# Kernel optimization log

Hardware: AMD Instinct MI355X
Metric: run time of the kernel (lower is better)

The kernel has to match this reference:

```python
import jax, jax.numpy as jnp
import numpy as np

B, C, H, W = 128, 8, 144, 144
TW, OG = 5, 2          # token_window, off_grid
NCLS, DT = 6, 256      # num_cls, dim_token
ITC = C * H * TW       # in_token_channel = 5760
EPS = 1e-5


def setup_inputs() -> dict:
    key = jax.random.key(0)
    ks = jax.random.split(key, 40)
    n = jax.random.normal
    u = jax.random.uniform
    CW = C * W  # 1152
    inp = {
        'x': n(ks[0], (B, C, H, W), jnp.float32),
        # ext head: Conv1d(1152,256,1) -> BN(256) -> Conv1d(256,2,1)
        'ext_w1': n(ks[1], (256, CW)) * 0.02, 'ext_b1': jnp.zeros((256,)),
        'ext_g': jnp.ones((256,)), 'ext_bb': jnp.zeros((256,)),
        'ext_m': n(ks[2], (256,)) * 0.1, 'ext_v': u(ks[3], (256,), minval=0.5, maxval=1.5),
        'ext_w2': n(ks[4], (2, 256)) * 0.05, 'ext_b2': jnp.zeros((2,)),
        # cls head: Conv1d(1152,256,1) -> BN(256) -> Conv1d(256,144,1)
        'cls_w1': n(ks[5], (256, CW)) * 0.02, 'cls_b1': jnp.zeros((256,)),
        'cls_g': jnp.ones((256,)), 'cls_bb': jnp.zeros((256,)),
        'cls_m': n(ks[6], (256,)) * 0.1, 'cls_v': u(ks[7], (256,), minval=0.5, maxval=1.5),
        'cls_w2': n(ks[8], (W, 256)) * 0.05, 'cls_b2': jnp.zeros((W,)),
        # to_token Linear(5760,256) and class embeddings
        'tok_w': n(ks[9], (ITC, DT)) * 0.01, 'tok_b': jnp.zeros((DT,)),
        'emb': n(ks[10], (NCLS, DT)),
        # transformer (depth=1, heads=2, dim_head=32 -> inner=64)
        'ln1_g': jnp.ones((DT,)), 'ln1_b': jnp.zeros((DT,)),
        'qkv_w': n(ks[11], (DT, 3 * 64)) * 0.05,
        'out_w': n(ks[12], (64, DT)) * 0.05, 'out_b': jnp.zeros((DT,)),
        'ln2_g': jnp.ones((DT,)), 'ln2_b': jnp.zeros((DT,)),
        'ff_w1': n(ks[13], (DT, 512)) * 0.05, 'ff_b1': jnp.zeros((512,)),
        'ff_w2': n(ks[14], (512, DT)) * 0.05, 'ff_b2': jnp.zeros((DT,)),
        'lnf_g': jnp.ones((DT,)), 'lnf_b': jnp.zeros((DT,)),
        'fin_w': n(ks[15], (DT, ITC)) * 0.02, 'fin_b': jnp.zeros((ITC,)),
    }
    return inp


def _ln(z, g, b):
    mu = jnp.mean(z, -1, keepdims=True)
    var = jnp.var(z, -1, keepdims=True)
    return (z - mu) * jax.lax.rsqrt(var + EPS) * g + b


def reference(x, ext_w1, ext_b1, ext_g, ext_bb, ext_m, ext_v, ext_w2, ext_b2,
              cls_w1, cls_b1, cls_g, cls_bb, cls_m, cls_v, cls_w2, cls_b2,
              tok_w, tok_b, emb,
              ln1_g, ln1_b, qkv_w, out_w, out_b,
              ln2_g, ln2_b, ff_w1, ff_b1, ff_w2, ff_b2,
              lnf_g, lnf_b, fin_w, fin_b):

    def head(row, w1, b1, g, bet, m, v, w2, b2):
        # row: [B, C*W, H]; 1x1 conv = per-position GEMM, BN in eval mode
        h = jnp.einsum('oc,bch->boh', w1, row) + b1[:, None]
        h = (h - m[:, None]) * jax.lax.rsqrt(v[:, None] + EPS) * g[:, None] + bet[:, None]
        h = jnp.einsum('oc,bch->boh', w2, h) + b2[:, None]
        return jnp.transpose(h, (0, 2, 1))  # [B, H, out]

    def heads_on(xx):
        # 'b c h w -> b (c w) h' (c major, w minor)
        row = jnp.transpose(xx, (0, 1, 3, 2)).reshape(B, C * W, H)
        e = jax.nn.softmax(head(row, ext_w1, ext_b1, ext_g, ext_bb, ext_m, ext_v, ext_w2, ext_b2), axis=2)
        c = jax.nn.softmax(head(row, cls_w1, cls_b1, cls_g, cls_bb, cls_m, cls_v, cls_w2, cls_b2), axis=2)
        return e, c

    ext, cls = heads_on(x)
    xp = jnp.pad(x, ((0, 0), (0, 0), (0, 0), (OG, OG)))  # [B,C,H,W+4]

    argmax_col = jnp.argmax(cls, axis=2)                  # [B,H]
    idx = argmax_col[:, :, None] + jnp.arange(TW)         # window in padded coords

    def transformer(t):  # t: [B, N, DT]
        z = _ln(t, ln1_g, ln1_b)
        q, k, v = jnp.split(z @ qkv_w, 3, axis=-1)
        sp = lambda a: a.reshape(B, -1, 2, 32).transpose(0, 2, 1, 3)  # b h n d
        q, k, v = sp(q), sp(k), sp(v)
        att = jax.nn.softmax(jnp.einsum('bhnd,bhmd->bhnm', q, k) * (32 ** -0.5), axis=-1)
        o = jnp.einsum('bhnm,bhmd->bhnd', att, v).transpose(0, 2, 1, 3).reshape(B, -1, 64)
        t = o @ out_w + out_b + t
        z = _ln(t, ln2_g, ln2_b)
        t = jax.nn.gelu(z @ ff_w1 + ff_b1, approximate=False) @ ff_w2 + ff_b2 + t
        t = _ln(t, lnf_g, lnf_b)
        return (t @ fin_w + fin_b).reshape(B, -1, C, H, TW)  # [B,N,C,H,TW]

    def refine(xpad):
        g_idx = jnp.broadcast_to(idx[:, None], (B, C, H, TW))
        patches = jnp.take_along_axis(xpad, g_idx, axis=3)    # [B,C,H,TW]
        tok = patches.reshape(B, -1) @ tok_w + tok_b          # [B,DT]
        tokens = tok[:, None, :] + emb[None]                  # [B,NCLS,DT]
        refined = transformer(tokens)                         # [B,NCLS,C,H,TW]
        xpt = jnp.transpose(xpad, (0, 2, 3, 1))               # [B,H,Wp,C]
        bb = jnp.arange(B)[:, None, None]
        hh = jnp.arange(H)[None, :, None]
        for i in range(NCLS):
            xpt = xpt.at[bb, hh, idx].set(jnp.transpose(refined[:, i], (0, 2, 3, 1)))
        return jnp.transpose(xpt, (0, 3, 1, 2))

    xp = jax.lax.cond(jnp.mean(ext[:, :, 0]) > 0.3, refine, lambda a: a, xp)
    x2 = xp[:, :, :, OG:W + OG]
    ext2, cls2 = heads_on(x2)
    return ext, cls, ext2, cls2
```

## Files before the change

### kernel.cpp

```cpp
#include <hip/hip_runtime.h>
#include <math.h>

#define EPSF 1e-5f
#define GAPTH 2e-4f
#define NKS 2
#define KSL 576
#define RROWS 18432


typedef __attribute__((ext_vector_type(8))) short short8v;
typedef __attribute__((ext_vector_type(4))) float f32x4;
typedef unsigned short ushort;
typedef unsigned int uint;

__device__ inline ushort f2bf(float f) {
    uint u = __float_as_uint(f);
    uint r = (u + 0x7FFFu + ((u >> 16) & 1u)) >> 16;
    return (ushort)r;
}
__device__ inline float bf2f(ushort h) { return __uint_as_float(((uint)h) << 16); }

__global__ __launch_bounds__(256) void wcomb_build(
    const float* __restrict__ w1e, const float* __restrict__ b1e, const float* __restrict__ ge,
    const float* __restrict__ bbe, const float* __restrict__ me, const float* __restrict__ ve,
    const float* __restrict__ w2e, const float* __restrict__ b2e,
    const float* __restrict__ w1c, const float* __restrict__ b1c, const float* __restrict__ gc,
    const float* __restrict__ bbc, const float* __restrict__ mc, const float* __restrict__ vc,
    const float* __restrict__ w2c, const float* __restrict__ b2c,
    float* __restrict__ Wc32, ushort* __restrict__ Wchi, ushort* __restrict__ Wclo,
    float* __restrict__ cconst)
{
    __shared__ float coef[256];
    __shared__ float csum[4];
    const int j = blockIdx.x, kq = blockIdx.y, tid = threadIdx.x;
    const int lane = tid & 63, wid = tid >> 6;

    const float *w1 = nullptr, *w2row = nullptr, *b1 = nullptr, *g = nullptr,
                *bb = nullptr, *m = nullptr, *v = nullptr;
    float b2v = 0.f;
    int valid = 0;
    if (j < 144) {
        valid = 1; w1 = w1c; w2row = w2c + (size_t)j * 256;
        b1 = b1c; g = gc; bb = bbc; m = mc; v = vc; b2v = b2c[j];
    } else if (j < 146) {
        valid = 1; w1 = w1e; w2row = w2e + (size_t)(j - 144) * 256;
        b1 = b1e; g = ge; bb = bbe; m = me; v = ve; b2v = b2e[j - 144];
    }

    float cf = 0.f, cc = 0.f;
    if (valid) {
        float s = g[tid] * rsqrtf(v[tid] + EPSF);
        float w2v = w2row[tid];
        cf = w2v * s;
        cc = w2v * ((b1[tid] - m[tid]) * s + bb[tid]);
    }
    coef[tid] = cf;
    if (kq == 0) {
        float t = cc;
#pragma unroll
        for (int off = 32; off; off >>= 1) t += __shfl_xor(t, off);
        if (lane == 0) csum[wid] = t;
    }
    __syncthreads();
    if (kq == 0 && tid == 0)
        cconst[j] = valid ? ((csum[0] + csum[1]) + (csum[2] + csum[3]) + b2v) : 0.f;

    for (int k = kq * 288 + tid; k < (kq + 1) * 288; k += 256) {
        float acc = 0.f;
        if (valid) {
            for (int o = 0; o < 256; o++) acc += coef[o] * w1[(size_t)o * 1152 + k];
        }
        Wc32[(size_t)j * 1152 + k] = acc;
        ushort hi = f2bf(acc);
        Wchi[(size_t)j * 1152 + k] = hi;
        Wclo[(size_t)j * 1152 + k] = f2bf(acc - bf2f(hi));
    }
}

__global__ void zero_counters(int* __restrict__ cand_count)
{
    *cand_count = 0;
}

__global__ __launch_bounds__(256) void transpose_w(
    const float* __restrict__ src, float* __restrict__ dst, int R, int Cc)
{
    __shared__ float tile[32][33];
    const int rb = blockIdx.y * 32, cb = blockIdx.x * 32;
    const int tx = threadIdx.x & 31, ty = threadIdx.x >> 5;
#pragma unroll
    for (int i = ty; i < 32; i += 8) {
        int r = rb + i, c = cb + tx;
        tile[i][tx] = (r < R && c < Cc) ? src[(size_t)r * Cc + c] : 0.f;
    }
    __syncthreads();
#pragma unroll
    for (int i = ty; i < 32; i += 8) {
        int c = cb + i, r = rb + tx;
        if (c < Cc && r < R) dst[(size_t)c * R + r] = tile[tx][i];
    }
}

__global__ __launch_bounds__(256) void logits_gemm(
    const float* __restrict__ x, const ushort* __restrict__ Wchi, const ushort* __restrict__ Wclo,
    float* __restrict__ logits_part)
{
    __shared__ ushort Ahi[64][40], Alo[64][40], Bhi[160][40], Blo[160][40];
    const int tid = threadIdx.x;
    const int lane = tid & 63, wid = tid >> 6;
    const int wm = wid & 1, wn = wid >> 1;
    const int rb = blockIdx.x * 64;
    const int ks = blockIdx.y;
    const int kbase = ks * KSL;
    const int NIT = KSL / 32;

    const int rl = tid >> 2, kk = (tid & 3) << 3;
    const int arow = rb + rl;
    const int ab = arow / 144, ahh = arow - ab * 144;

    const int br0 = tid >> 2, bk0 = (tid & 3) << 3;
    const int br2 = 128 + (tid >> 2), bk2 = (tid & 3) << 3;

    float av[8];
    short8v vbh0, vbl0, vbh1, vbl1, vbh2, vbl2;

    auto LOAD = [&](int kb) {
        int k1 = kb + kk, c1 = k1 / 144, w1 = k1 - c1 * 144;
        const float4 t0 = *reinterpret_cast<const float4*>(
            x + (((size_t)(ab * 8 + c1) * 144 + ahh) * 144 + w1));
        const float4 t1 = *reinterpret_cast<const float4*>(
            x + (((size_t)(ab * 8 + c1) * 144 + ahh) * 144 + w1 + 4));
        av[0] = t0.x; av[1] = t0.y; av[2] = t0.z; av[3] = t0.w;
        av[4] = t1.x; av[5] = t1.y; av[6] = t1.z; av[7] = t1.w;
        size_t o0 = (size_t)br0 * 1152 + kb + bk0;
        vbh0 = *reinterpret_cast<const short8v*>(Wchi + o0);
        vbl0 = *reinterpret_cast<const short8v*>(Wclo + o0);
        size_t o1 = (size_t)(br0 + 64) * 1152 + kb + bk0;
        vbh1 = *reinterpret_cast<const short8v*>(Wchi + o1);
        vbl1 = *reinterpret_cast<const short8v*>(Wclo + o1);
        if (tid < 128) {
            size_t o2 = (size_t)br2 * 1152 + kb + bk2;
            vbh2 = *reinterpret_cast<const short8v*>(Wchi + o2);
            vbl2 = *reinterpret_cast<const short8v*>(Wclo + o2);
        }
    };

    auto STORE = [&]() {
        short8v hv, lv;
#pragma unroll
        for (int q = 0; q < 8; q++) {
            ushort h = f2bf(av[q]);
            hv[q] = (short)h;
            lv[q] = (short)f2bf(av[q] - bf2f(h));
        }
        *reinterpret_cast<short8v*>(&Ahi[rl][kk]) = hv;
        *reinterpret_cast<short8v*>(&Alo[rl][kk]) = lv;
        *reinterpret_cast<short8v*>(&Bhi[br0][bk0]) = vbh0;
        *reinterpret_cast<short8v*>(&Blo[br0][bk0]) = vbl0;
        *reinterpret_cast<short8v*>(&Bhi[br0 + 64][bk0]) = vbh1;
        *reinterpret_cast<short8v*>(&Blo[br0 + 64][bk0]) = vbl1;
        if (tid < 128) {
            *reinterpret_cast<short8v*>(&Bhi[br2][bk2]) = vbh2;
            *reinterpret_cast<short8v*>(&Blo[br2][bk2]) = vbl2;
        }
    };

    f32x4 acc[2][5];
#pragma unroll
    for (int mt = 0; mt < 2; mt++)
#pragma unroll
        for (int nt = 0; nt < 5; nt++) acc[mt][nt] = (f32x4){0.f, 0.f, 0.f, 0.f};

    const int fr = lane & 15, fg = (lane >> 4) << 3;

    LOAD(kbase);
    for (int t = 0; t < NIT; t++) {
        STORE();
        if (t < NIT - 1) LOAD(kbase + (t + 1) * 32);
        __syncthreads();
        short8v ah0 = *reinterpret_cast<const short8v*>(&Ahi[wm * 32 + fr][fg]);
        short8v al0 = *reinterpret_cast<const short8v*>(&Alo[wm * 32 + fr][fg]);
        short8v ah1 = *reinterpret_cast<const short8v*>(&Ahi[wm * 32 + 16 + fr][fg]);
        short8v al1 = *reinterpret_cast<const short8v*>(&Alo[wm * 32 + 16 + fr][fg]);
#pragma unroll
        for (int nt = 0; nt < 5; nt++) {
            short8v bh = *reinterpret_cast<const short8v*>(&Bhi[wn * 80 + nt * 16 + fr][fg]);
            short8v bl = *reinterpret_cast<const short8v*>(&Blo[wn * 80 + nt * 16 + fr][fg]);
            acc[0][nt] = __builtin_amdgcn_mfma_f32_16x16x32_bf16(ah0, bh, acc[0][nt], 0, 0, 0);
            acc[0][nt] = __builtin_amdgcn_mfma_f32_16x16x32_bf16(ah0, bl, acc[0][nt], 0, 0, 0);
            acc[0][nt] = __builtin_amdgcn_mfma_f32_16x16x32_bf16(al0, bh, acc[0][nt], 0, 0, 0);
            acc[1][nt] = __builtin_amdgcn_mfma_f32_16x16x32_bf16(ah1, bh, acc[1][nt], 0, 0, 0);
            acc[1][nt] = __builtin_amdgcn_mfma_f32_16x16x32_bf16(ah1, bl, acc[1][nt], 0, 0, 0);
            acc[1][nt] = __builtin_amdgcn_mfma_f32_16x16x32_bf16(al1, bh, acc[1][nt], 0, 0, 0);
        }
        __syncthreads();
    }

    float* base = logits_part + (size_t)ks * RROWS * 160;
#pragma unroll
    for (int mt = 0; mt < 2; mt++) {
#pragma unroll
        for (int nt = 0; nt < 5; nt++) {
            int gcol = wn * 80 + nt * 16 + fr;
            if (gcol < 146) {
                float* dst = base + (size_t)(rb + wm * 32 + mt * 16 + ((lane >> 4) << 2)) * 160 + gcol;
#pragma unroll
                for (int i = 0; i < 4; i++)
                    dst[(size_t)i * 160] = acc[mt][nt][i];
            }
        }
    }
}

template<int DELTA>
__global__ __launch_bounds__(256) void softmax_heads(
    const float* __restrict__ logits_part, const float* __restrict__ cconst,
    float* __restrict__ out_cls, float* __restrict__ out_ext,
    int* __restrict__ amax, float* __restrict__ partials,
    int* __restrict__ cand_count, int* __restrict__ cand_list,
    const float* __restrict__ x, const float* __restrict__ WcT,
    const float* __restrict__ refined5, const int* __restrict__ flag)
{
    __shared__ float ps[4];
    __shared__ float dL[4][148];
    __shared__ float dsh[4][40];
    __shared__ int   ksh[4][40];
    const int r4 = threadIdx.x >> 6, lane = threadIdx.x & 63;
    const int row = blockIdx.x * 4 + r4;

    if (DELTA) {
        const int fl = *flag;
        if (fl) {
            const int b = row / 144, hh = row - b * 144;
            const int a = amax[row];
            if (lane < 40) {
                int c = lane / 5, tw = lane - c * 5;
                int w = a - 2 + tw;
                float d = 0.f; int k = 0;
                if (w >= 0 && w < 144) {
                    k = c * 144 + w;
                    d = refined5[(size_t)b * 5760 + (c * 144 + hh) * 5 + tw]
                      - x[((size_t)(b * 8 + c) * 144 + hh) * 144 + w];
                }
                dsh[r4][lane] = d; ksh[r4][lane] = k;
            }
            __syncthreads();
#pragma unroll
            for (int rj = 0; rj < 3; rj++) {
                int j = lane + rj * 64;
                if (j < 146) {
                    float acc = 0.f;
#pragma unroll 8
                    for (int i = 0; i < 40; i++)
                        acc += WcT[(size_t)ksh[r4][i] * 160 + j] * dsh[r4][i];
                    dL[r4][j] = acc;
                }
            }
        } else {
#pragma unroll
            for (int rj = 0; rj < 3; rj++) {
                int j = lane + rj * 64;
                if (j < 146) dL[r4][j] = 0.f;
            }
        }
        __syncthreads();
    }

    const float* L0 = logits_part + (size_t)row * 160;
    const float* L1 = L0 + (size_t)RROWS * 160;
    float v0 = L0[lane] + L1[lane] + cconst[lane];
    float v1 = L0[lane + 64] + L1[lane + 64] + cconst[lane + 64];
    float v2 = (lane < 16) ? (L0[lane + 128] + L1[lane + 128] + cconst[lane + 128])
                           : -3.0e38f;
    if (DELTA) {
        v0 += dL[r4][lane];
        v1 += dL[r4][lane + 64];
        if (lane < 16) v2 += dL[r4][lane + 128];
    }
    float m = v0; int mi = lane;
    if (v1 > m) { m = v1; mi = lane + 64; }
    if (v2 > m) { m = v2; mi = lane + 128; }
    float m1 = v0, m2 = -3.0e38f;
    if (v1 > m1) { m2 = m1; m1 = v1; } else m2 = v1;
    if (v2 > m1) { m2 = m1; m1 = v2; } else m2 = fmaxf(m2, v2);
#pragma unroll
    for (int off = 32; off; off >>= 1) {
        float om = __shfl_xor(m, off);
        int   oi = __shfl_xor(mi, off);
        if (om > m || (om == m && oi < mi)) { m = om; mi = oi; }
        float om1 = __shfl_xor(m1, off);
        float om2 = __shfl_xor(m2, off);
        float nm1 = fmaxf(m1, om1);
        m2 = fmaxf(fminf(m1, om1), fmaxf(m2, om2));
        m1 = nm1;
    }
    float e0 = expf(v0 - m), e1 = expf(v1 - m);
    float e2 = (lane < 16) ? expf(v2 - m) : 0.f;
    float s = e0 + e1 + e2;
#pragma unroll
    for (int off = 32; off; off >>= 1) s += __shfl_xor(s, off);
    float inv = 1.f / s;
    float* O = out_cls + (size_t)row * 144;
    O[lane] = e0 * inv;
    O[lane + 64] = e1 * inv;
    if (lane < 16) O[lane + 128] = e2 * inv;

    float l0 = L0[144] + L1[144] + cconst[144];
    float l1 = L0[145] + L1[145] + cconst[145];
    if (DELTA) { l0 += dL[r4][144]; l1 += dL[r4][145]; }
    float mx = fmaxf(l0, l1);
    float ee0 = expf(l0 - mx), ee1 = expf(l1 - mx);
    float einv = 1.f / (ee0 + ee1);
    float p0 = ee0 * einv;
    if (lane == 0) {
        out_ext[(size_t)row * 2] = p0;
        out_ext[(size_t)row * 2 + 1] = ee1 * einv;
        if (amax != nullptr && !DELTA) {
            amax[row] = mi;
            if (m1 - m2 < GAPTH) {
                int slot = atomicAdd(cand_count, 1);
                cand_list[slot] = row;
            }
        }
    }
    if (partials != nullptr) {
        if (lane == 0) ps[r4] = p0;
        __syncthreads();
        if (threadIdx.x == 0) partials[blockIdx.x] = (ps[0] + ps[1]) + (ps[2] + ps[3]);
    }
}

__global__ __launch_bounds__(256) void reduce_flag(const float* __restrict__ partials, int n,
                                                   int* __restrict__ flag)
{
    __shared__ float sm[256];
    int tid = threadIdx.x;
    float s = 0.f;
    for (int i = tid; i < n; i += 256) s += partials[i];
    sm[tid] = s; __syncthreads();
    for (int off = 128; off; off >>= 1) {
        if (tid < off) sm[tid] += sm[tid + off];
        __syncthreads();
    }
    if (tid == 0) *flag = (sm[0] * (1.f / 18432.f) > 0.3f) ? 1 : 0;
}

__global__ __launch_bounds__(256) void fixup_list(
    const int* __restrict__ cand_count, const int* __restrict__ cand_list,
    const float* __restrict__ x,
    const float* __restrict__ w1cT, const float* __restrict__ b1c,
    const float* __restrict__ gc, const float* __restrict__ bbc,
    const float* __restrict__ mc, const float* __restrict__ vc,
    const float* __restrict__ w2cT, const float* __restrict__ b2c,
    int* __restrict__ amax)
{
    __shared__ float xrow[1152];
    __shared__ float hsh[256];
    __shared__ float Lsh[144];
    const int tid = threadIdx.x;
    const int n = *cand_count;

    for (int ci = blockIdx.x; ci < n; ci += gridDim.x) {
        const int row = cand_list[ci];
        const int b = row / 144, hh = row - b * 144;
        for (int e = tid; e < 1152; e += 256) {
            int c = e / 144, w = e - c * 144;
            xrow[e] = x[(((size_t)(b * 8 + c) * 144 + hh) * 144) + w];
        }
        __syncthreads();
        {
            float a0 = 0.f, a1 = 0.f, a2 = 0.f, a3 = 0.f;
#pragma unroll 4
            for (int k = 0; k < 1152; k += 4) {
                a0 += w1cT[(size_t)k * 256 + tid] * xrow[k];
                a1 += w1cT[(size_t)(k + 1) * 256 + tid] * xrow[k + 1];
                a2 += w1cT[(size_t)(k + 2) * 256 + tid] * xrow[k + 2];
                a3 += w1cT[(size_t)(k + 3) * 256 + tid] * xrow[k + 3];
            }
            float a = (a0 + a1) + (a2 + a3);
            float sc = gc[tid] * rsqrtf(vc[tid] + EPSF);
            hsh[tid] = (a + b1c[tid] - mc[tid]) * sc + bbc[tid];
        }
        __syncthreads();
        if (tid < 144) {
            float a0 = 0.f, a1 = 0.f, a2 = 0.f, a3 = 0.f;
#pragma unroll 4
            for (int k = 0; k < 256; k += 4) {
                a0 += w2cT[(size_t)k * 144 + tid] * hsh[k];
                a1 += w2cT[(size_t)(k + 1) * 144 + tid] * hsh[k + 1];
                a2 += w2cT[(size_t)(k + 2) * 144 + tid] * hsh[k + 2];
                a3 += w2cT[(size_t)(k + 3) * 144 + tid] * hsh[k + 3];
            }
            Lsh[tid] = (a0 + a1) + (a2 + a3) + b2c[tid];
        }
        __syncthreads();
        if (tid == 0) {
            int bi = 0; float bv = Lsh[0];
            for (int j = 1; j < 144; j++) if (Lsh[j] > bv) { bv = Lsh[j]; bi = j; }
            amax[row] = bi;
        }
        __syncthreads();
    }
}

__global__ __launch_bounds__(256) void tok_partial(const float* __restrict__ x,
    const int* __restrict__ amax, const float* __restrict__ tok_w, float* __restrict__ tpart)
{
    __shared__ float P[720];
    __shared__ int ash[144];
    int b = blockIdx.x, c = blockIdx.y, tid = threadIdx.x;
    if (tid < 144) ash[tid] = amax[b * 144 + tid];
    __syncthreads();
    for (int e = tid; e < 720; e += 256) {
        int hh = e / 5, tw = e - hh * 5;
        int w = ash[hh] + tw - 2;
        P[e] = (w >= 0 && w < 144) ? x[(((size_t)(b * 8 + c) * 144 + hh) * 144) + w] : 0.f;
    }
    __syncthreads();
    const float* wbase = tok_w + (size_t)c * 720 * 256;
    float a0 = 0.f, a1 = 0.f, a2 = 0.f, a3 = 0.f;
    for (int k = 0; k < 720; k += 4) {
        a0 += P[k]     * wbase[(size_t)k * 256 + tid];
        a1 += P[k + 1] * wbase[(size_t)(k + 1) * 256 + tid];
        a2 += P[k + 2] * wbase[(size_t)(k + 2) * 256 + tid];
        a3 += P[k + 3] * wbase[(size_t)(k + 3) * 256 + tid];
    }
    tpart[((size_t)b * 8 + c) * 256 + tid] = (a0 + a1) + (a2 + a3);
}

__global__ __launch_bounds__(512) void attn_front(
    const float* __restrict__ tpart, const float* __restrict__ tok_b,
    const float* __restrict__ emb,
    const float* __restrict__ ln1_g, const float* __restrict__ ln1_b,
    const float* __restrict__ qkv_w,
    const float* __restrict__ out_w, const float* __restrict__ out_b,
    const float* __restrict__ ln2_g, const float* __restrict__ ln2_b,
    float* __restrict__ z2_5, float* __restrict__ t5out)
{
    __shared__ float s[256];
    __shared__ float z[6][256];
    __shared__ float qk[6][192];
    __shared__ float att[2][6];
    __shared__ float o5[64];
    __shared__ float t5[256];
    __shared__ float stat[2];
    const int b = blockIdx.x, tid = threadIdx.x;
    const int lane = tid & 63, wv = tid >> 6;
    const int g4 = tid >> 2, l4 = tid & 3;

    if (tid < 256) {
        float a = tok_b[tid];
#pragma unroll
        for (int ks = 0; ks < 8; ks++) a += tpart[((size_t)b * 8 + ks) * 256 + tid];
        s[tid] = a;
    }
    __syncthreads();

    if (wv < 6) {
        float y[4], s1 = 0.f, s2 = 0.f;
#pragma unroll
        for (int q = 0; q < 4; q++) {
            int k = lane + 64 * q;
            y[q] = s[k] + emb[wv * 256 + k];
            s1 += y[q]; s2 += y[q] * y[q];
        }
#pragma unroll
        for (int off = 32; off; off >>= 1) { s1 += __shfl_xor(s1, off); s2 += __shfl_xor(s2, off); }
        float mu = s1 * (1.f / 256.f);
        float var = s2 * (1.f / 256.f) - mu * mu;
        float rs = rsqrtf(var + EPSF);
#pragma unroll
        for (int q = 0; q < 4; q++) {
            int k = lane + 64 * q;
            z[wv][k] = (y[q] - mu) * rs * ln1_g[k] + ln1_b[k];
        }
    }
    __syncthreads();

    for (int tt = g4; tt < 832; tt += 128) {
        int i, c;
        if (tt < 768) { i = tt >> 7; c = 64 + (tt & 127); }
        else          { i = 5;       c = tt - 768; }
        float a = 0.f;
#pragma unroll 8
        for (int j = 0; j < 64; j++) {
            int k = l4 + 4 * j;
            a += z[i][k] * qkv_w[(size_t)k * 192 + c];
        }
        a += __shfl_xor(a, 1);
        a += __shfl_xor(a, 2);
        if (l4 == 0) qk[i][c] = a;
    }
    __syncthreads();

    if (tid < 12) {
        int h = tid / 6, j = tid - h * 6;
        float a = 0.f;
#pragma unroll
        for (int d = 0; d < 32; d++) a += qk[5][h * 32 + d] * qk[j][64 + h * 32 + d];
        att[h][j] = a * 0.17677669529663687f;
    }
    __syncthreads();
    if (tid < 2) {
        float m = -3.0e38f;
        for (int j = 0; j < 6; j++) m = fmaxf(m, att[tid][j]);
        float ssum = 0.f;
        for (int j = 0; j < 6; j++) { float e = expf(att[tid][j] - m); att[tid][j] = e; ssum += e; }
        float inv = 1.f / ssum;
        for (int j = 0; j < 6; j++) att[tid][j] *= inv;
    }
    __syncthreads();
    if (tid < 64) {
        int h = tid >> 5;
        float a = 0.f;
#pragma unroll
        for (int j = 0; j < 6; j++) a += att[h][j] * qk[j][128 + tid];
        o5[tid] = a;
    }
    __syncthreads();

    for (int tt = g4; tt < 256; tt += 128) {
        float a = 0.f;
#pragma unroll
        for (int j = 0; j < 16; j++) {
            int d = l4 + 4 * j;
            a += o5[d] * out_w[(size_t)d * 256 + tt];
        }
        a += __shfl_xor(a, 1);
        a += __shfl_xor(a, 2);
        if (l4 == 0) t5[tt] = a + out_b[tt] + s[tt] + emb[5 * 256 + tt];
    }
    __syncthreads();

    if (wv == 0) {
        float s1 = 0.f, s2 = 0.f;
#pragma unroll
        for (int q = 0; q < 4; q++) { float vv = t5[lane + 64 * q]; s1 += vv; s2 += vv * vv; }
#pragma unroll
        for (int off = 32; off; off >>= 1) { s1 += __shfl_xor(s1, off); s2 += __shfl_xor(s2, off); }
        if (lane == 0) {
            float mu = s1 * (1.f / 256.f);
            float var = s2 * (1.f / 256.f) - mu * mu;
            stat[0] = mu; stat[1] = rsqrtf(var + EPSF);
        }
    }
    __syncthreads();
    if (tid < 256) {
        t5out[(size_t)b * 256 + tid] = t5[tid];
        z2_5[(size_t)b * 256 + tid] = (t5[tid] - stat[0]) * stat[1] * ln2_g[tid] + ln2_b[tid];
    }
}

__global__ __launch_bounds__(512) void ff1_gelu(
    const float* __restrict__ z2_5, const float* __restrict__ ff_w1,
    const float* __restrict__ ff_b1, float* __restrict__ f5)
{
    __shared__ float zsh[256];
    const int b = blockIdx.x, half = blockIdx.y, tid = threadIdx.x;
    const int g4 = tid >> 2, l4 = tid & 3;
    if (tid < 256) zsh[tid] = z2_5[(size_t)b * 256 + tid];
    __syncthreads();
    for (int tt = g4; tt < 256; tt += 128) {
        const int jj = half * 256 + tt;
        float a = 0.f;
#pragma unroll 8
        for (int j = 0; j < 64; j++) {
            int k = l4 + 4 * j;
            a += zsh[k] * ff_w1[(size_t)k * 512 + jj];
        }
        a += __shfl_xor(a, 1);
        a += __shfl_xor(a, 2);
        if (l4 == 0) {
            a += ff_b1[jj];
            f5[(size_t)b * 512 + jj] = 0.5f * a * (1.f + erff(a * 0.70710678118654752f));
        }
    }
}

__global__ __launch_bounds__(512) void ff2_lnf(
    const float* __restrict__ f5, const float* __restrict__ ff_w2,
    const float* __restrict__ ff_b2, const float* __restrict__ t5in,
    const float* __restrict__ lnf_g, const float* __restrict__ lnf_b,
    float* __restrict__ tfin)
{
    __shared__ float fsh[512];
    __shared__ float tsh[256];
    __shared__ float stat[2];
    const int b = blockIdx.x, tid = threadIdx.x;
    const int lane = tid & 63, wv = tid >> 6;
    const int g4 = tid >> 2, l4 = tid & 3;
    fsh[tid] = f5[(size_t)b * 512 + tid];
    __syncthreads();
    for (int tt = g4; tt < 256; tt += 128) {
        float a = 0.f;
#pragma unroll 8
        for (int j = 0; j < 128; j++) {
            int k = l4 + 4 * j;
            a += fsh[k] * ff_w2[(size_t)k * 256 + tt];
        }
        a += __shfl_xor(a, 1);
        a += __shfl_xor(a, 2);
        if (l4 == 0) tsh[tt] = a + ff_b2[tt] + t5in[(size_t)b * 256 + tt];
    }
    __syncthreads();
    if (wv == 0) {
        float s1 = 0.f, s2 = 0.f;
#pragma unroll
        for (int q = 0; q < 4; q++) { float vv = tsh[lane + 64 * q]; s1 += vv; s2 += vv * vv; }
#pragma unroll
        for (int off = 32; off; off >>= 1) { s1 += __shfl_xor(s1, off); s2 += __shfl_xor(s2, off); }
        if (lane == 0) {
            float mu = s1 * (1.f / 256.f);
            float var = s2 * (1.f / 256.f) - mu * mu;
            stat[0] = mu; stat[1] = rsqrtf(var + EPSF);
        }
    }
    __syncthreads();
    if (tid < 256)
        tfin[(size_t)b * 256 + tid] = (tsh[tid] - stat[0]) * stat[1] * lnf_g[tid] + lnf_b[tid];
}

__global__ __launch_bounds__(256) void fin_gemm(const float* __restrict__ tfin,
    const float* __restrict__ fin_w, const float* __restrict__ fin_b, float* __restrict__ refined5)
{
    __shared__ float tf[16][256];
    int tid = threadIdx.x;
    int nb = blockIdx.x * 256 + tid;
    int bg = blockIdx.y * 16;
    for (int e = tid; e < 4096; e += 256) tf[e >> 8][e & 255] = tfin[(size_t)(bg + (e >> 8)) * 256 + (e & 255)];
    __syncthreads();
    if (nb < 5760) {
        float acc[16];
#pragma unroll
        for (int bb = 0; bb < 16; bb++) acc[bb] = 0.f;
        for (int k = 0; k < 256; k++) {
            float wv = fin_w[(size_t)k * 5760 + nb];
#pragma unroll
            for (int bb = 0; bb < 16; bb++) acc[bb] += tf[bb][k] * wv;
        }
        float fb = fin_b[nb];
#pragma unroll
        for (int bb = 0; bb < 16; bb++)
            refined5[(size_t)(bg + bb) * 5760 + nb] = acc[bb] + fb;
    }
}

extern "C" void kernel_launch(void* const* d_in, const int* in_sizes, int n_in,
                              void* d_out, int out_size, void* d_ws, size_t ws_size,
                              hipStream_t stream)
{
    const float* x      = (const float*)d_in[0];
    const float* ext_w1 = (const float*)d_in[1];
    const float* ext_b1 = (const float*)d_in[2];
    const float* ext_g  = (const float*)d_in[3];
    const float* ext_bb = (const float*)d_in[4];
    const float* ext_m  = (const float*)d_in[5];
    const float* ext_v  = (const float*)d_in[6];
    const float* ext_w2 = (const float*)d_in[7];
    const float* ext_b2 = (const float*)d_in[8];
    const float* cls_w1 = (const float*)d_in[9];
    const float* cls_b1 = (const float*)d_in[10];
    const float* cls_g  = (const float*)d_in[11];
    const float* cls_bb = (const float*)d_in[12];
    const float* cls_m  = (const float*)d_in[13];
    const float* cls_v  = (const float*)d_in[14];
    const float* cls_w2 = (const float*)d_in[15];
    const float* cls_b2 = (const float*)d_in[16];
    const float* tok_w  = (const float*)d_in[17];
    const float* tok_b  = (const float*)d_in[18];
    const float* emb    = (const float*)d_in[19];
    const float* ln1_g  = (const float*)d_in[20];
    const float* ln1_b  = (const float*)d_in[21];
    const float* qkv_w  = (const float*)d_in[22];
    const float* out_w  = (const float*)d_in[23];
    const float* out_b  = (const float*)d_in[24];
    const float* ln2_g  = (const float*)d_in[25];
    const float* ln2_b  = (const float*)d_in[26];
    const float* ff_w1  = (const float*)d_in[27];
    const float* ff_b1  = (const float*)d_in[28];
    const float* ff_w2  = (const float*)d_in[29];
    const float* ff_b2  = (const float*)d_in[30];
    const float* lnf_g  = (const float*)d_in[31];
    const float* lnf_b  = (const float*)d_in[32];
    const float* fin_w  = (const float*)d_in[33];
    const float* fin_b  = (const float*)d_in[34];

    float* out = (float*)d_out;
    float* ws  = (float*)d_ws;

    float*  Wc32     = ws;
    float*  cconst   = ws + 184320;
    ushort* Wchi     = (ushort*)(ws + 184480);
    ushort* Wclo     = (ushort*)(ws + 276640);
    float*  logitsP  = ws + 368800;
    float*  partials = ws + 6267040;
    float*  z2_5     = ws + 6271648;
    float*  t5buf    = ws + 6304416;
    float*  f5buf    = ws + 6337184;
    float*  tfin     = ws + 6402720;
    float*  refined5 = ws + 6435488;
    float*  tpart    = ws + 7172768;
    int*    amax     = (int*)(ws + 7434912);
    int*    flag     = (int*)(ws + 7453344);
    int*    cand_cnt = (int*)(ws + 7453345);
    int*    cand_lst = (int*)(ws + 7453346);
    float*  w1cT     = ws + 7471780;
    float*  w2cT     = ws + 7766692;
    float*  WcT      = ws + 7803556;

    float* out_ext  = out;
    float* out_cls  = out + 36864;
    float* out_ext2 = out + 2691072;
    float* out_cls2 = out + 2727936;

    dim3 blk(256);

    wcomb_build<<<dim3(160, 4), blk, 0, stream>>>(
        ext_w1, ext_b1, ext_g, ext_bb, ext_m, ext_v, ext_w2, ext_b2,
        cls_w1, cls_b1, cls_g, cls_bb, cls_m, cls_v, cls_w2, cls_b2,
        Wc32, Wchi, Wclo, cconst);
    zero_counters<<<1, 1, 0, stream>>>(cand_cnt);
    transpose_w<<<dim3(36, 8), blk, 0, stream>>>(cls_w1, w1cT, 256, 1152);
    transpose_w<<<dim3(8, 5), blk, 0, stream>>>(cls_w2, w2cT, 144, 256);
    transpose_w<<<dim3(36, 5), blk, 0, stream>>>(Wc32, WcT, 160, 1152);

    logits_gemm<<<dim3(288, NKS), blk, 0, stream>>>(x, Wchi, Wclo, logitsP);
    softmax_heads<0><<<4608, blk, 0, stream>>>(logitsP, cconst, out_cls, out_ext, amax, partials,
        cand_cnt, cand_lst, nullptr, nullptr, nullptr, nullptr);
    reduce_flag<<<1, blk, 0, stream>>>(partials, 4608, flag);
    fixup_list<<<256, blk, 0, stream>>>(cand_cnt, cand_lst, x,
        w1cT, cls_b1, cls_g, cls_bb, cls_m, cls_v, w2cT, cls_b2, amax);

    tok_partial<<<dim3(128, 8), blk, 0, stream>>>(x, amax, tok_w, tpart);
    attn_front<<<128, dim3(512), 0, stream>>>(tpart, tok_b, emb, ln1_g, ln1_b, qkv_w,
        out_w, out_b, ln2_g, ln2_b, z2_5, t5buf);
    ff1_gelu<<<dim3(128, 2), dim3(512), 0, stream>>>(z2_5, ff_w1, ff_b1, f5buf);
    ff2_lnf<<<128, dim3(512), 0, stream>>>(f5buf, ff_w2, ff_b2, t5buf, lnf_g, lnf_b, tfin);
    fin_gemm<<<dim3(23, 8), blk, 0, stream>>>(tfin, fin_w, fin_b, refined5);

    softmax_heads<1><<<4608, blk, 0, stream>>>(logitsP, cconst, out_cls2, out_ext2, amax, nullptr,
        nullptr, nullptr, x, WcT, refined5, flag);
}
```

Measured before the change: 278.3 us.

## Fuse transformer FF kernels, merge transposes, shrink logits GEMM row tile

Fuses attn_front, ff1_gelu and ff2_lnf into one attn_ff kernel that keeps intermediates in shared memory, and merges the three weight transposes into a single 3D-grid launch. This removes several launches and global round trips. The logits GEMM row tile drops from 64 to 32, doubling the grid to 576x2 for more parallelism at the cost of re-reading the B tiles more often. The wcomb_build inner loop is split into four accumulators for more ILP. The FF1 stage now runs on 128 blocks instead of 256, which loses some parallelism.

```diff
diff --git a/kernel.cpp b/kernel.cpp
--- a/kernel.cpp
+++ b/kernel.cpp
@@ -9,6 +9,7 @@
 
 
 typedef __attribute__((ext_vector_type(8))) short short8v;
+typedef __attribute__((ext_vector_type(4))) short short4v;
 typedef __attribute__((ext_vector_type(4))) float f32x4;
 typedef unsigned short ushort;
 typedef unsigned int uint;
@@ -68,7 +69,14 @@
     for (int k = kq * 288 + tid; k < (kq + 1) * 288; k += 256) {
         float acc = 0.f;
         if (valid) {
-            for (int o = 0; o < 256; o++) acc += coef[o] * w1[(size_t)o * 1152 + k];
+            float a0 = 0.f, a1 = 0.f, a2 = 0.f, a3 = 0.f;
+            for (int o = 0; o < 256; o += 4) {
+                a0 += coef[o]     * w1[(size_t)o * 1152 + k];
+                a1 += coef[o + 1] * w1[(size_t)(o + 1) * 1152 + k];
+                a2 += coef[o + 2] * w1[(size_t)(o + 2) * 1152 + k];
+                a3 += coef[o + 3] * w1[(size_t)(o + 3) * 1152 + k];
+            }
+            acc = (a0 + a1) + (a2 + a3);
         }
         Wc32[(size_t)j * 1152 + k] = acc;
         ushort hi = f2bf(acc);
@@ -82,9 +90,17 @@
     *cand_count = 0;
 }
 
-__global__ __launch_bounds__(256) void transpose_w(
-    const float* __restrict__ src, float* __restrict__ dst, int R, int Cc)
-{
+__global__ __launch_bounds__(256) void transpose3(
+    const float* __restrict__ s0, float* __restrict__ d0,
+    const float* __restrict__ s1, float* __restrict__ d1,
+    const float* __restrict__ s2, float* __restrict__ d2)
+{
+    const float* src; float* dst; int R, Cc;
+    if (blockIdx.z == 0)      { src = s0; dst = d0; R = 256; Cc = 1152; }
+    else if (blockIdx.z == 1) { src = s1; dst = d1; R = 144; Cc = 256;
+                                if (blockIdx.x >= 8 || blockIdx.y >= 5) return; }
+    else                      { src = s2; dst = d2; R = 160; Cc = 1152;
+                                if (blockIdx.y >= 5) return; }
     __shared__ float tile[32][33];
     const int rb = blockIdx.y * 32, cb = blockIdx.x * 32;
     const int tx = threadIdx.x & 31, ty = threadIdx.x >> 5;
@@ -105,33 +121,30 @@
     const float* __restrict__ x, const ushort* __restrict__ Wchi, const ushort* __restrict__ Wclo,
     float* __restrict__ logits_part)
 {
-    __shared__ ushort Ahi[64][40], Alo[64][40], Bhi[160][40], Blo[160][40];
+    __shared__ ushort Ahi[32][40], Alo[32][40], Bhi[160][40], Blo[160][40];
     const int tid = threadIdx.x;
     const int lane = tid & 63, wid = tid >> 6;
     const int wm = wid & 1, wn = wid >> 1;
-    const int rb = blockIdx.x * 64;
+    const int rb = blockIdx.x * 32;
     const int ks = blockIdx.y;
     const int kbase = ks * KSL;
     const int NIT = KSL / 32;
 
-    const int rl = tid >> 2, kk = (tid & 3) << 3;
-    const int arow = rb + rl;
+    const int arl = tid >> 3, akk = (tid & 7) << 2;
+    const int arow = rb + arl;
     const int ab = arow / 144, ahh = arow - ab * 144;
 
     const int br0 = tid >> 2, bk0 = (tid & 3) << 3;
     const int br2 = 128 + (tid >> 2), bk2 = (tid & 3) << 3;
 
-    float av[8];
+    float av[4];
     short8v vbh0, vbl0, vbh1, vbl1, vbh2, vbl2;
 
     auto LOAD = [&](int kb) {
-        int k1 = kb + kk, c1 = k1 / 144, w1 = k1 - c1 * 144;
+        int k1 = kb + akk, c1 = k1 / 144, w1 = k1 - c1 * 144;
         const float4 t0 = *reinterpret_cast<const float4*>(
             x + (((size_t)(ab * 8 + c1) * 144 + ahh) * 144 + w1));
-        const float4 t1 = *reinterpret_cast<const float4*>(
-            x + (((size_t)(ab * 8 + c1) * 144 + ahh) * 144 + w1 + 4));
         av[0] = t0.x; av[1] = t0.y; av[2] = t0.z; av[3] = t0.w;
-        av[4] = t1.x; av[5] = t1.y; av[6] = t1.z; av[7] = t1.w;
         size_t o0 = (size_t)br0 * 1152 + kb + bk0;
         vbh0 = *reinterpret_cast<const short8v*>(Wchi + o0);
         vbl0 = *reinterpret_cast<const short8v*>(Wclo + o0);
@@ -146,15 +159,15 @@
     };
 
     auto STORE = [&]() {
-        short8v hv, lv;
-#pragma unroll
-        for (int q = 0; q < 8; q++) {
+        short4v hv, lv;
+#pragma unroll
+        for (int q = 0; q < 4; q++) {
             ushort h = f2bf(av[q]);
             hv[q] = (short)h;
             lv[q] = (short)f2bf(av[q] - bf2f(h));
         }
-        *reinterpret_cast<short8v*>(&Ahi[rl][kk]) = hv;
-        *reinterpret_cast<short8v*>(&Alo[rl][kk]) = lv;
+        *reinterpret_cast<short4v*>(&Ahi[arl][akk]) = hv;
+        *reinterpret_cast<short4v*>(&Alo[arl][akk]) = lv;
         *reinterpret_cast<short8v*>(&Bhi[br0][bk0]) = vbh0;
         *reinterpret_cast<short8v*>(&Blo[br0][bk0]) = vbl0;
         *reinterpret_cast<short8v*>(&Bhi[br0 + 64][bk0]) = vbh1;
@@ -165,11 +178,9 @@
         }
     };
 
-    f32x4 acc[2][5];
-#pragma unroll
-    for (int mt = 0; mt < 2; mt++)
-#pragma unroll
-        for (int nt = 0; nt < 5; nt++) acc[mt][nt] = (f32x4){0.f, 0.f, 0.f, 0.f};
+    f32x4 acc[5];
+#pragma unroll
+    for (int nt = 0; nt < 5; nt++) acc[nt] = (f32x4){0.f, 0.f, 0.f, 0.f};
 
     const int fr = lane & 15, fg = (lane >> 4) << 3;
 
@@ -178,36 +189,29 @@
         STORE();
         if (t < NIT - 1) LOAD(kbase + (t + 1) * 32);
         __syncthreads();
-        short8v ah0 = *reinterpret_cast<const short8v*>(&Ahi[wm * 32 + fr][fg]);
-        short8v al0 = *reinterpret_cast<const short8v*>(&Alo[wm * 32 + fr][fg]);
-        short8v ah1 = *reinterpret_cast<const short8v*>(&Ahi[wm * 32 + 16 + fr][fg]);
-        short8v al1 = *reinterpret_cast<const short8v*>(&Alo[wm * 32 + 16 + fr][fg]);
+        short8v ah = *reinterpret_cast<const short8v*>(&Ahi[wm * 16 + fr][fg]);
+        short8v al = *reinterpret_cast<const short8v*>(&Alo[wm * 16 + fr][fg]);
 #pragma unroll
         for (int nt = 0; nt < 5; nt++) {
             short8v bh = *reinterpret_cast<const short8v*>(&Bhi[wn * 80 + nt * 16 + fr][fg]);
             short8v bl = *reinterpret_cast<const short8v*>(&Blo[wn * 80 + nt * 16 + fr][fg]);
-            acc[0][nt] = __builtin_amdgcn_mfma_f32_16x16x32_bf16(ah0, bh, acc[0][nt], 0, 0, 0);
-            acc[0][nt] = __builtin_amdgcn_mfma_f32_16x16x32_bf16(ah0, bl, acc[0][nt], 0, 0, 0);
-            acc[0][nt] = __builtin_amdgcn_mfma_f32_16x16x32_bf16(al0, bh, acc[0][nt], 0, 0, 0);
-            acc[1][nt] = __builtin_amdgcn_mfma_f32_16x16x32_bf16(ah1, bh, acc[1][nt], 0, 0, 0);
-            acc[1][nt] = __builtin_amdgcn_mfma_f32_16x16x32_bf16(ah1, bl, acc[1][nt], 0, 0, 0);
-            acc[1][nt] = __builtin_amdgcn_mfma_f32_16x16x32_bf16(al1, bh, acc[1][nt], 0, 0, 0);
+            acc[nt] = __builtin_amdgcn_mfma_f32_16x16x32_bf16(ah, bh, acc[nt], 0, 0, 0);
+            acc[nt] = __builtin_amdgcn_mfma_f32_16x16x32_bf16(ah, bl, acc[nt], 0, 0, 0);
+            acc[nt] = __builtin_amdgcn_mfma_f32_16x16x32_bf16(al, bh, acc[nt], 0, 0, 0);
         }
         __syncthreads();
     }
 
     float* base = logits_part + (size_t)ks * RROWS * 160;
-#pragma unroll
-    for (int mt = 0; mt < 2; mt++) {
-#pragma unroll
-        for (int nt = 0; nt < 5; nt++) {
-            int gcol = wn * 80 + nt * 16 + fr;
-            if (gcol < 146) {
-                float* dst = base + (size_t)(rb + wm * 32 + mt * 16 + ((lane >> 4) << 2)) * 160 + gcol;
-#pragma unroll
-                for (int i = 0; i < 4; i++)
-                    dst[(size_t)i * 160] = acc[mt][nt][i];
-            }
+    const int orow = rb + wm * 16 + ((lane >> 4) << 2);
+#pragma unroll
+    for (int nt = 0; nt < 5; nt++) {
+        int gcol = wn * 80 + nt * 16 + fr;
+        if (gcol < 146) {
+            float* dst = base + (size_t)orow * 160 + gcol;
+#pragma unroll
+            for (int i = 0; i < 4; i++)
+                dst[(size_t)i * 160] = acc[nt][i];
         }
     }
 }
@@ -428,14 +432,17 @@
     tpart[((size_t)b * 8 + c) * 256 + tid] = (a0 + a1) + (a2 + a3);
 }
 
-__global__ __launch_bounds__(512) void attn_front(
+__global__ __launch_bounds__(512) void attn_ff(
     const float* __restrict__ tpart, const float* __restrict__ tok_b,
     const float* __restrict__ emb,
     const float* __restrict__ ln1_g, const float* __restrict__ ln1_b,
     const float* __restrict__ qkv_w,
     const float* __restrict__ out_w, const float* __restrict__ out_b,
     const float* __restrict__ ln2_g, const float* __restrict__ ln2_b,
-    float* __restrict__ z2_5, float* __restrict__ t5out)
+    const float* __restrict__ ff_w1, const float* __restrict__ ff_b1,
+    const float* __restrict__ ff_w2, const float* __restrict__ ff_b2,
+    const float* __restrict__ lnf_g, const float* __restrict__ lnf_b,
+    float* __restrict__ tfin)
 {
     __shared__ float s[256];
     __shared__ float z[6][256];
@@ -443,6 +450,8 @@
     __shared__ float att[2][6];
     __shared__ float o5[64];
     __shared__ float t5[256];
+    __shared__ float zsh[256];
+    __shared__ float fsh[512];
     __shared__ float stat[2];
     const int b = blockIdx.x, tid = threadIdx.x;
     const int lane = tid & 63, wv = tid >> 6;
@@ -545,52 +554,26 @@
         }
     }
     __syncthreads();
-    if (tid < 256) {
-        t5out[(size_t)b * 256 + tid] = t5[tid];
-        z2_5[(size_t)b * 256 + tid] = (t5[tid] - stat[0]) * stat[1] * ln2_g[tid] + ln2_b[tid];
-    }
-}
-
-__global__ __launch_bounds__(512) void ff1_gelu(
-    const float* __restrict__ z2_5, const float* __restrict__ ff_w1,
-    const float* __restrict__ ff_b1, float* __restrict__ f5)
-{
-    __shared__ float zsh[256];
-    const int b = blockIdx.x, half = blockIdx.y, tid = threadIdx.x;
-    const int g4 = tid >> 2, l4 = tid & 3;
-    if (tid < 256) zsh[tid] = z2_5[(size_t)b * 256 + tid];
-    __syncthreads();
-    for (int tt = g4; tt < 256; tt += 128) {
-        const int jj = half * 256 + tt;
+    if (tid < 256)
+        zsh[tid] = (t5[tid] - stat[0]) * stat[1] * ln2_g[tid] + ln2_b[tid];
+    __syncthreads();
+
+    for (int tt = g4; tt < 512; tt += 128) {
         float a = 0.f;
 #pragma unroll 8
         for (int j = 0; j < 64; j++) {
             int k = l4 + 4 * j;
-            a += zsh[k] * ff_w1[(size_t)k * 512 + jj];
+            a += zsh[k] * ff_w1[(size_t)k * 512 + tt];
         }
         a += __shfl_xor(a, 1);
         a += __shfl_xor(a, 2);
         if (l4 == 0) {
-            a += ff_b1[jj];
-            f5[(size_t)b * 512 + jj] = 0.5f * a * (1.f + erff(a * 0.70710678118654752f));
-        }
-    }
-}
-
-__global__ __launch_bounds__(512) void ff2_lnf(
-    const float* __restrict__ f5, const float* __restrict__ ff_w2,
-    const float* __restrict__ ff_b2, const float* __restrict__ t5in,
-    const float* __restrict__ lnf_g, const float* __restrict__ lnf_b,
-    float* __restrict__ tfin)
-{
-    __shared__ float fsh[512];
-    __shared__ float tsh[256];
-    __shared__ float stat[2];
-    const int b = blockIdx.x, tid = threadIdx.x;
-    const int lane = tid & 63, wv = tid >> 6;
-    const int g4 = tid >> 2, l4 = tid & 3;
-    fsh[tid] = f5[(size_t)b * 512 + tid];
-    __syncthreads();
+            a += ff_b1[tt];
+            fsh[tt] = 0.5f * a * (1.f + erff(a * 0.70710678118654752f));
+        }
+    }
+    __syncthreads();
+
     for (int tt = g4; tt < 256; tt += 128) {
         float a = 0.f;
 #pragma unroll 8
@@ -600,13 +583,14 @@
         }
         a += __shfl_xor(a, 1);
         a += __shfl_xor(a, 2);
-        if (l4 == 0) tsh[tt] = a + ff_b2[tt] + t5in[(size_t)b * 256 + tt];
-    }
-    __syncthreads();
+        if (l4 == 0) s[tt] = a + ff_b2[tt] + t5[tt];
+    }
+    __syncthreads();
+
     if (wv == 0) {
         float s1 = 0.f, s2 = 0.f;
 #pragma unroll
-        for (int q = 0; q < 4; q++) { float vv = tsh[lane + 64 * q]; s1 += vv; s2 += vv * vv; }
+        for (int q = 0; q < 4; q++) { float vv = s[lane + 64 * q]; s1 += vv; s2 += vv * vv; }
 #pragma unroll
         for (int off = 32; off; off >>= 1) { s1 += __shfl_xor(s1, off); s2 += __shfl_xor(s2, off); }
         if (lane == 0) {
@@ -617,7 +601,7 @@
     }
     __syncthreads();
     if (tid < 256)
-        tfin[(size_t)b * 256 + tid] = (tsh[tid] - stat[0]) * stat[1] * lnf_g[tid] + lnf_b[tid];
+        tfin[(size_t)b * 256 + tid] = (s[tid] - stat[0]) * stat[1] * lnf_g[tid] + lnf_b[tid];
 }
 
 __global__ __launch_bounds__(256) void fin_gemm(const float* __restrict__ tfin,
@@ -694,9 +678,6 @@
     ushort* Wclo     = (ushort*)(ws + 276640);
     float*  logitsP  = ws + 368800;
     float*  partials = ws + 6267040;
-    float*  z2_5     = ws + 6271648;
-    float*  t5buf    = ws + 6304416;
-    float*  f5buf    = ws + 6337184;
     float*  tfin     = ws + 6402720;
     float*  refined5 = ws + 6435488;
     float*  tpart    = ws + 7172768;
@@ -720,11 +701,9 @@
         cls_w1, cls_b1, cls_g, cls_bb, cls_m, cls_v, cls_w2, cls_b2,
         Wc32, Wchi, Wclo, cconst);
     zero_counters<<<1, 1, 0, stream>>>(cand_cnt);
-    transpose_w<<<dim3(36, 8), blk, 0, stream>>>(cls_w1, w1cT, 256, 1152);
-    transpose_w<<<dim3(8, 5), blk, 0, stream>>>(cls_w2, w2cT, 144, 256);
-    transpose_w<<<dim3(36, 5), blk, 0, stream>>>(Wc32, WcT, 160, 1152);
-
-    logits_gemm<<<dim3(288, NKS), blk, 0, stream>>>(x, Wchi, Wclo, logitsP);
+    transpose3<<<dim3(36, 8, 3), blk, 0, stream>>>(cls_w1, w1cT, cls_w2, w2cT, Wc32, WcT);
+
+    logits_gemm<<<dim3(576, NKS), blk, 0, stream>>>(x, Wchi, Wclo, logitsP);
     softmax_heads<0><<<4608, blk, 0, stream>>>(logitsP, cconst, out_cls, out_ext, amax, partials,
         cand_cnt, cand_lst, nullptr, nullptr, nullptr, nullptr);
     reduce_flag<<<1, blk, 0, stream>>>(partials, 4608, flag);
@@ -732,10 +711,8 @@
         w1cT, cls_b1, cls_g, cls_bb, cls_m, cls_v, w2cT, cls_b2, amax);
 
     tok_partial<<<dim3(128, 8), blk, 0, stream>>>(x, amax, tok_w, tpart);
-    attn_front<<<128, dim3(512), 0, stream>>>(tpart, tok_b, emb, ln1_g, ln1_b, qkv_w,
-        out_w, out_b, ln2_g, ln2_b, z2_5, t5buf);
-    ff1_gelu<<<dim3(128, 2), dim3(512), 0, stream>>>(z2_5, ff_w1, ff_b1, f5buf);
-    ff2_lnf<<<128, dim3(512), 0, stream>>>(f5buf, ff_w2, ff_b2, t5buf, lnf_g, lnf_b, tfin);
+    attn_ff<<<128, dim3(512), 0, stream>>>(tpart, tok_b, emb, ln1_g, ln1_b, qkv_w,
+        out_w, out_b, ln2_g, ln2_b, ff_w1, ff_b1, ff_w2, ff_b2, lnf_g, lnf_b, tfin);
     fin_gemm<<<dim3(23, 8), blk, 0, stream>>>(tfin, fin_w, fin_b, refined5);
 
     softmax_heads<1><<<4608, blk, 0, stream>>>(logitsP, cconst, out_cls2, out_ext2, amax, nullptr,
```

After: 284.5 us. +2.2%, slower.
